# Kernel tuning notes

Measured on AMD Instinct MI355X. Metric: run time of the kernel, lower is better.

The kernel has to match this reference:

```python
import jax, jax.numpy as jnp
import numpy as np


def setup_inputs() -> dict:
    key = jax.random.key(0)
    k1, k2 = jax.random.split(key)
    TOKENS, IN, OUT = 32768, 1024, 1024
    x = jax.random.normal(k1, (TOKENS, IN), dtype=jnp.float32)
    # weight init: uniform(-1, 1) over [out_features, in_features]
    weight = jax.random.uniform(k2, (OUT, IN), dtype=jnp.float32, minval=-1.0, maxval=1.0)
    b = jnp.zeros((OUT,), dtype=jnp.float32)
    return {"x": x, "weight": weight, "b": b}


def reference(x, weight, b):
    # ternary quantization: sign() zeros out exact zeros; mask keeps nonzeros
    sign = jnp.sign(weight)
    mask = (weight != 0).astype(x.dtype)
    w_q = sign * mask  # [out, in], values in {-1, 0, 1}
    # F.linear: x @ w_q.T + b
    return jnp.einsum("ti,oi->to", x, w_q) + b
```

## Files before the change

kernel.cpp:

```cpp
#include <hip/hip_runtime.h>
#include <hip/hip_bf16.h>


typedef __bf16 bf16x8 __attribute__((ext_vector_type(8)));
typedef float  f32x4  __attribute__((ext_vector_type(4)));

#define BM 128
#define BN 128
#define BK 32

__device__ __forceinline__ void async16(const void* gptr, void* lptr) {
    __builtin_amdgcn_global_load_lds(
        (const __attribute__((address_space(1))) unsigned int*)gptr,
        (__attribute__((address_space(3))) unsigned int*)lptr,
        16, 0, 0);
}


__global__ void cvt_x_bf16(const float* __restrict__ in, __bf16* __restrict__ out, long n) {
    long i = ((long)blockIdx.x * blockDim.x + threadIdx.x) * 8;
    if (i + 8 > n) return;
    const float4* p = (const float4*)(in + i);
    float4 a = p[0];
    float4 b = p[1];
    bf16x8 v;
    v[0] = (__bf16)a.x; v[1] = (__bf16)a.y; v[2] = (__bf16)a.z; v[3] = (__bf16)a.w;
    v[4] = (__bf16)b.x; v[5] = (__bf16)b.y; v[6] = (__bf16)b.z; v[7] = (__bf16)b.w;
    *(bf16x8*)(out + i) = v;
}

__device__ __forceinline__ float signf(float v) {
    return (v > 0.0f) ? 1.0f : ((v < 0.0f) ? -1.0f : 0.0f);
}

__global__ void cvt_w_sign(const float* __restrict__ in, __bf16* __restrict__ out, long n) {
    long i = ((long)blockIdx.x * blockDim.x + threadIdx.x) * 8;
    if (i + 8 > n) return;
    const float4* p = (const float4*)(in + i);
    float4 a = p[0];
    float4 b = p[1];
    bf16x8 v;
    v[0] = (__bf16)signf(a.x); v[1] = (__bf16)signf(a.y);
    v[2] = (__bf16)signf(a.z); v[3] = (__bf16)signf(a.w);
    v[4] = (__bf16)signf(b.x); v[5] = (__bf16)signf(b.y);
    v[6] = (__bf16)signf(b.z); v[7] = (__bf16)signf(b.w);
    *(bf16x8*)(out + i) = v;
}


__global__ __launch_bounds__(256)
void gemm_bt(const __bf16* __restrict__ A, const __bf16* __restrict__ B,
             const float* __restrict__ bias, float* __restrict__ C,
             int M, int N, int K) {
    __shared__ __align__(16) __bf16 sA[BM * BK];
    __shared__ __align__(16) __bf16 sB[BN * BK];

    const int tid  = threadIdx.x;
    const int lane = tid & 63;
    const int wave = tid >> 6;

    const int bm = blockIdx.y * BM;
    const int bn = blockIdx.x * BN;

    const int wrow = (wave >> 1) * 64;
    const int wcol = (wave & 1) * 64;

    const int quad = lane >> 4;
    const int l16  = lane & 15;

    f32x4 acc[4][4] = {};

    const int row0 = tid >> 2;
    const int col8 = (tid & 3) * 8;

    for (int k0 = 0; k0 < K; k0 += BK) {
        {
            const __bf16* ga0 = A + (long)(bm + row0) * K + k0 + col8;
            const __bf16* ga1 = A + (long)(bm + 64 + row0) * K + k0 + col8;
            const __bf16* gb0 = B + (long)(bn + row0) * K + k0 + col8;
            const __bf16* gb1 = B + (long)(bn + 64 + row0) * K + k0 + col8;
            async16(ga0, (char*)sA + tid * 16);
            async16(ga1, (char*)sA + (256 + tid) * 16);
            async16(gb0, (char*)sB + tid * 16);
            async16(gb1, (char*)sB + (256 + tid) * 16);
        }
        __syncthreads();

        bf16x8 af[4], bfr[4];
#pragma unroll
        for (int i = 0; i < 4; ++i) {
            af[i]  = *(const bf16x8*)&sA[(wrow + i * 16 + l16) * BK + quad * 8];
            bfr[i] = *(const bf16x8*)&sB[(wcol + i * 16 + l16) * BK + quad * 8];
        }
#pragma unroll
        for (int i = 0; i < 4; ++i)
#pragma unroll
            for (int j = 0; j < 4; ++j)
                acc[i][j] = __builtin_amdgcn_mfma_f32_16x16x32_bf16(af[i], bfr[j], acc[i][j], 0, 0, 0);

        __syncthreads();
    }

#pragma unroll
    for (int j = 0; j < 4; ++j) {
        const int col = bn + wcol + j * 16 + l16;
        const float bv = bias[col];
#pragma unroll
        for (int i = 0; i < 4; ++i) {
            const int rbase = bm + wrow + i * 16 + quad * 4;
#pragma unroll
            for (int r = 0; r < 4; ++r) {
                C[(long)(rbase + r) * N + col] = acc[i][j][r] + bv;
            }
        }
    }
}


__global__ void fallback_kernel(const float* __restrict__ x, const float* __restrict__ w,
                                const float* __restrict__ b, float* __restrict__ out,
                                int M, int N, int K) {
    long o = (long)blockIdx.x * blockDim.x + threadIdx.x;
    if (o >= (long)M * N) return;
    int t = (int)(o / N);
    int n = (int)(o % N);
    const float* xr = x + (long)t * K;
    const float* wr = w + (long)n * K;
    float s = 0.0f;
    for (int k = 0; k < K; ++k) {
        s += xr[k] * signf(wr[k]);
    }
    out[o] = s + b[n];
}


extern "C" void kernel_launch(void* const* d_in, const int* in_sizes, int n_in,
                              void* d_out, int out_size, void* d_ws, size_t ws_size,
                              hipStream_t stream) {
    const float* x = (const float*)d_in[0];
    const float* w = (const float*)d_in[1];
    const float* b = (const float*)d_in[2];
    float* out = (float*)d_out;

    const int N = in_sizes[2];
    const int K = in_sizes[1] / N;
    const int M = in_sizes[0] / K;

    const size_t nx = (size_t)M * K;
    const size_t nw = (size_t)N * K;
    const size_t need = (nx + nw) * sizeof(__bf16);

    const bool fast = (M % BM == 0) && (N % BN == 0) && (K % BK == 0) &&
                      (nx % 2048 == 0) && (nw % 2048 == 0) && (ws_size >= need);

    if (!fast) {
        long total = (long)M * N;
        int blocks = (int)((total + 255) / 256);
        fallback_kernel<<<blocks, 256, 0, stream>>>(x, w, b, out, M, N, K);
        return;
    }

    __bf16* xb = (__bf16*)d_ws;
    __bf16* wb = xb + nx;

    cvt_x_bf16<<<(int)(nx / 2048), 256, 0, stream>>>(x, xb, (long)nx);
    cvt_w_sign<<<(int)(nw / 2048), 256, 0, stream>>>(w, wb, (long)nw);

    dim3 grid(N / BN, M / BM);
    gemm_bt<<<grid, 256, 0, stream>>>(xb, wb, b, out, M, N, K);
}
```

Baseline: 329.8 us.

## Switch GEMM to int8 MFMA with per-row activation quantization

The bf16 conversion path is replaced by one fused pre-pass. It quantizes each activation row to int8 using a per-row absmax scale and packs the ternary weights as int8. The GEMM now uses the i32 16x16x64 int8 MFMA with a 64-wide K tile, an XCD-aware block swizzle and per-row rescaling in the epilogue. This halves operand bytes and K-loop iterations, at the cost of coarser activation precision than bf16.

```diff
diff --git a/kernel.cpp b/kernel.cpp
--- a/kernel.cpp
+++ b/kernel.cpp
@@ -2,12 +2,12 @@
 #include <hip/hip_bf16.h>
 
 
-typedef __bf16 bf16x8 __attribute__((ext_vector_type(8)));
-typedef float  f32x4  __attribute__((ext_vector_type(4)));
+typedef int   i32x4 __attribute__((ext_vector_type(4)));
+typedef float f32x4 __attribute__((ext_vector_type(4)));
 
 #define BM 128
 #define BN 128
-#define BK 32
+#define BK 64
 
 __device__ __forceinline__ void async16(const void* gptr, void* lptr) {
     __builtin_amdgcn_global_load_lds(
@@ -16,87 +16,133 @@
         16, 0, 0);
 }
 
-
-__global__ void cvt_x_bf16(const float* __restrict__ in, __bf16* __restrict__ out, long n) {
-    long i = ((long)blockIdx.x * blockDim.x + threadIdx.x) * 8;
-    if (i + 8 > n) return;
-    const float4* p = (const float4*)(in + i);
-    float4 a = p[0];
-    float4 b = p[1];
-    bf16x8 v;
-    v[0] = (__bf16)a.x; v[1] = (__bf16)a.y; v[2] = (__bf16)a.z; v[3] = (__bf16)a.w;
-    v[4] = (__bf16)b.x; v[5] = (__bf16)b.y; v[6] = (__bf16)b.z; v[7] = (__bf16)b.w;
-    *(bf16x8*)(out + i) = v;
-}
-
-__device__ __forceinline__ float signf(float v) {
-    return (v > 0.0f) ? 1.0f : ((v < 0.0f) ? -1.0f : 0.0f);
-}
-
-__global__ void cvt_w_sign(const float* __restrict__ in, __bf16* __restrict__ out, long n) {
-    long i = ((long)blockIdx.x * blockDim.x + threadIdx.x) * 8;
-    if (i + 8 > n) return;
-    const float4* p = (const float4*)(in + i);
-    float4 a = p[0];
-    float4 b = p[1];
-    bf16x8 v;
-    v[0] = (__bf16)signf(a.x); v[1] = (__bf16)signf(a.y);
-    v[2] = (__bf16)signf(a.z); v[3] = (__bf16)signf(a.w);
-    v[4] = (__bf16)signf(b.x); v[5] = (__bf16)signf(b.y);
-    v[6] = (__bf16)signf(b.z); v[7] = (__bf16)signf(b.w);
-    *(bf16x8*)(out + i) = v;
+__device__ __forceinline__ int clamp127(int v) {
+    v = v > 127 ? 127 : v;
+    v = v < -127 ? -127 : v;
+    return v;
+}
+
+__device__ __forceinline__ int pack4(int a, int b, int c, int d) {
+    return (a & 255) | ((b & 255) << 8) | ((c & 255) << 16) | ((d & 255) << 24);
+}
+
+__device__ __forceinline__ int sgnb(float v) {
+    return (v > 0.0f) ? 1 : ((v < 0.0f) ? -1 : 0);
 }
 
 
 __global__ __launch_bounds__(256)
-void gemm_bt(const __bf16* __restrict__ A, const __bf16* __restrict__ B,
-             const float* __restrict__ bias, float* __restrict__ C,
-             int M, int N, int K) {
-    __shared__ __align__(16) __bf16 sA[BM * BK];
-    __shared__ __align__(16) __bf16 sB[BN * BK];
+void quant_pre(const float* __restrict__ x, const float* __restrict__ w,
+               signed char* __restrict__ xq, signed char* __restrict__ wq,
+               float* __restrict__ scales, int M, int K, long nw, int xblocks) {
+    const int tid = threadIdx.x;
+
+    if ((int)blockIdx.x >= xblocks) {
+        long i = ((long)(blockIdx.x - xblocks) * 256 + tid) * 8;
+        if (i + 8 > nw) return;
+        const float4* p = (const float4*)(w + i);
+        float4 a = p[0];
+        float4 b = p[1];
+        int lo = pack4(sgnb(a.x), sgnb(a.y), sgnb(a.z), sgnb(a.w));
+        int hi = pack4(sgnb(b.x), sgnb(b.y), sgnb(b.z), sgnb(b.w));
+        int2 v; v.x = lo; v.y = hi;
+        *(int2*)(wq + i) = v;
+        return;
+    }
+
+    const int wv   = tid >> 6;
+    const int lane = tid & 63;
+    const int row  = blockIdx.x * 4 + wv;
+    if (row >= M) return;
+
+    const float* xr = x + (long)row * K;
+    const int chunks = K >> 8;
+    float4 v[8];
+    float m = 0.0f;
+#pragma unroll
+    for (int q = 0; q < 8; ++q) {
+        if (q >= chunks) break;
+        v[q] = *(const float4*)(xr + q * 256 + lane * 4);
+        m = fmaxf(m, fmaxf(fmaxf(fabsf(v[q].x), fabsf(v[q].y)),
+                           fmaxf(fabsf(v[q].z), fabsf(v[q].w))));
+    }
+#pragma unroll
+    for (int off = 32; off > 0; off >>= 1)
+        m = fmaxf(m, __shfl_xor(m, off, 64));
+
+    const float inv = (m > 0.0f) ? (127.0f / m) : 0.0f;
+    int* qr = (int*)(xq + (long)row * K);
+#pragma unroll
+    for (int q = 0; q < 8; ++q) {
+        if (q >= chunks) break;
+        int a = clamp127(__float2int_rn(v[q].x * inv));
+        int b = clamp127(__float2int_rn(v[q].y * inv));
+        int c = clamp127(__float2int_rn(v[q].z * inv));
+        int d = clamp127(__float2int_rn(v[q].w * inv));
+        qr[q * 64 + lane] = pack4(a, b, c, d);
+    }
+    if (lane == 0) scales[row] = m * (1.0f / 127.0f);
+}
+
+
+__global__ __launch_bounds__(256)
+void gemm_i8(const signed char* __restrict__ A, const signed char* __restrict__ B,
+             const float* __restrict__ scales, const float* __restrict__ bias,
+             float* __restrict__ C, int M, int N, int K, int swz) {
+    __shared__ __align__(16) signed char sA[BM * BK];
+    __shared__ __align__(16) signed char sB[BN * BK];
 
     const int tid  = threadIdx.x;
     const int lane = tid & 63;
     const int wave = tid >> 6;
 
-    const int bm = blockIdx.y * BM;
-    const int bn = blockIdx.x * BN;
+    const int gn = N / BN;
+    int mt, nt;
+    if (swz) {
+        const int b    = blockIdx.x;
+        const int xcd  = b & 7;
+        const int rest = b >> 3;
+        nt = rest % gn;
+        mt = (rest / gn) * 8 + xcd;
+    } else {
+        nt = blockIdx.x % gn;
+        mt = blockIdx.x / gn;
+    }
+    const int bm = mt * BM;
+    const int bn = nt * BN;
 
     const int wrow = (wave >> 1) * 64;
     const int wcol = (wave & 1) * 64;
-
     const int quad = lane >> 4;
     const int l16  = lane & 15;
 
-    f32x4 acc[4][4] = {};
-
-    const int row0 = tid >> 2;
-    const int col8 = (tid & 3) * 8;
+    i32x4 acc[4][4] = {};
+
+    const int row0  = tid >> 2;
+    const int col16 = (tid & 3) * 16;
+    const signed char* pa0 = A + (long)(bm + row0) * K + col16;
+    const signed char* pa1 = pa0 + (long)64 * K;
+    const signed char* pb0 = B + (long)(bn + row0) * K + col16;
+    const signed char* pb1 = pb0 + (long)64 * K;
 
     for (int k0 = 0; k0 < K; k0 += BK) {
-        {
-            const __bf16* ga0 = A + (long)(bm + row0) * K + k0 + col8;
-            const __bf16* ga1 = A + (long)(bm + 64 + row0) * K + k0 + col8;
-            const __bf16* gb0 = B + (long)(bn + row0) * K + k0 + col8;
-            const __bf16* gb1 = B + (long)(bn + 64 + row0) * K + k0 + col8;
-            async16(ga0, (char*)sA + tid * 16);
-            async16(ga1, (char*)sA + (256 + tid) * 16);
-            async16(gb0, (char*)sB + tid * 16);
-            async16(gb1, (char*)sB + (256 + tid) * 16);
+        async16(pa0 + k0, (char*)sA + tid * 16);
+        async16(pa1 + k0, (char*)sA + (256 + tid) * 16);
+        async16(pb0 + k0, (char*)sB + tid * 16);
+        async16(pb1 + k0, (char*)sB + (256 + tid) * 16);
+        __syncthreads();
+
+        i32x4 af[4], bfr[4];
+#pragma unroll
+        for (int i = 0; i < 4; ++i) {
+            af[i]  = *(const i32x4*)&sA[(wrow + i * 16 + l16) * BK + quad * 16];
+            bfr[i] = *(const i32x4*)&sB[(wcol + i * 16 + l16) * BK + quad * 16];
         }
-        __syncthreads();
-
-        bf16x8 af[4], bfr[4];
-#pragma unroll
-        for (int i = 0; i < 4; ++i) {
-            af[i]  = *(const bf16x8*)&sA[(wrow + i * 16 + l16) * BK + quad * 8];
-            bfr[i] = *(const bf16x8*)&sB[(wcol + i * 16 + l16) * BK + quad * 8];
-        }
 #pragma unroll
         for (int i = 0; i < 4; ++i)
 #pragma unroll
             for (int j = 0; j < 4; ++j)
-                acc[i][j] = __builtin_amdgcn_mfma_f32_16x16x32_bf16(af[i], bfr[j], acc[i][j], 0, 0, 0);
+                acc[i][j] = __builtin_amdgcn_mfma_i32_16x16x64_i8(af[i], bfr[j], acc[i][j], 0, 0, 0);
 
         __syncthreads();
     }
@@ -110,12 +156,17 @@
             const int rbase = bm + wrow + i * 16 + quad * 4;
 #pragma unroll
             for (int r = 0; r < 4; ++r) {
-                C[(long)(rbase + r) * N + col] = acc[i][j][r] + bv;
+                const int row = rbase + r;
+                C[(long)row * N + col] = (float)acc[i][j][r] * scales[row] + bv;
             }
         }
     }
 }
 
+
+__device__ __forceinline__ float signf(float v) {
+    return (v > 0.0f) ? 1.0f : ((v < 0.0f) ? -1.0f : 0.0f);
+}
 
 __global__ void fallback_kernel(const float* __restrict__ x, const float* __restrict__ w,
                                 const float* __restrict__ b, float* __restrict__ out,
@@ -127,9 +178,7 @@
     const float* xr = x + (long)t * K;
     const float* wr = w + (long)n * K;
     float s = 0.0f;
-    for (int k = 0; k < K; ++k) {
-        s += xr[k] * signf(wr[k]);
-    }
+    for (int k = 0; k < K; ++k) s += xr[k] * signf(wr[k]);
     out[o] = s + b[n];
 }
 
@@ -146,12 +195,13 @@
     const int K = in_sizes[1] / N;
     const int M = in_sizes[0] / K;
 
-    const size_t nx = (size_t)M * K;
-    const size_t nw = (size_t)N * K;
-    const size_t need = (nx + nw) * sizeof(__bf16);
+    const long nx = (long)M * K;
+    const long nw = (long)N * K;
+    const size_t need = (size_t)nx + (size_t)nw + (size_t)M * 4 + 64;
 
     const bool fast = (M % BM == 0) && (N % BN == 0) && (K % BK == 0) &&
-                      (nx % 2048 == 0) && (nw % 2048 == 0) && (ws_size >= need);
+                      (K % 256 == 0) && (K <= 2048) && (nw % 2048 == 0) &&
+                      (ws_size >= need);
 
     if (!fast) {
         long total = (long)M * N;
@@ -160,12 +210,15 @@
         return;
     }
 
-    __bf16* xb = (__bf16*)d_ws;
-    __bf16* wb = xb + nx;
-
-    cvt_x_bf16<<<(int)(nx / 2048), 256, 0, stream>>>(x, xb, (long)nx);
-    cvt_w_sign<<<(int)(nw / 2048), 256, 0, stream>>>(w, wb, (long)nw);
-
-    dim3 grid(N / BN, M / BM);
-    gemm_bt<<<grid, 256, 0, stream>>>(xb, wb, b, out, M, N, K);
-}
+    signed char* xq = (signed char*)d_ws;
+    signed char* wq = xq + nx;
+    float* scales   = (float*)(wq + nw);
+
+    const int xblocks = M / 4;
+    const int wblocks = (int)(nw / 2048);
+    quant_pre<<<xblocks + wblocks, 256, 0, stream>>>(x, w, xq, wq, scales, M, K, nw, xblocks);
+
+    const int gm = M / BM, gn = N / BN;
+    const int swz = (gm % 8 == 0) ? 1 : 0;
+    gemm_i8<<<gm * gn, 256, 0, stream>>>(xq, wq, scales, b, out, M, N, K, swz);
+}
```

New measurement: 286.5 us. -13.1%, faster.
